# Kernel optimization log

Hardware: AMD Instinct MI355X
Metric: run time of the kernel (lower is better)

Reference implementation:

```python
import jax, jax.numpy as jnp
import numpy as np

KH, KW = 3, 3  # window_size[1], window_size[2]
SH, SW = 1, 1  # strides
FILTERS = 64


def _extract_patches(x, kh, kw, sh, sw):
    # TF tf.image.extract_patches ordering: depth = (row, col, channel), channel fastest.
    B, H, W, C = x.shape
    Ho = (H - kh) // sh + 1
    Wo = (W - kw) // sw + 1
    # stack kh*kw shifted views -> (B, Ho, Wo, kh*kw, C)
    views = [x[:, i:i + (Ho - 1) * sh + 1:sh, j:j + (Wo - 1) * sw + 1:sw, :]
             for i in range(kh) for j in range(kw)]
    patches = jnp.stack(views, axis=3)
    return patches.reshape(B, Ho, Wo, kh * kw * C)


def setup_inputs() -> dict:
    key = jax.random.key(0)
    k1, k2 = jax.random.split(key)
    B, H, W, C = 8, 32, 32, 32
    K = KH * KW * C  # 288
    x = jax.random.normal(k1, (B, H, W, C), dtype=jnp.float32)
    w = jax.random.normal(k2, (1, 1, 1, K, FILTERS), dtype=jnp.float32) * 0.05
    bias = jnp.zeros((FILTERS,), dtype=jnp.float32)
    return {"x": x, "w": w, "bias": bias}


def reference(x, w, bias):
    # patches: (B, Ho, Wo, K)
    patches = _extract_patches(x, KH, KW, SH, SW)
    # broadcast add: (B, Ho, Wo, K, F)
    s = patches[..., None] + w
    # tropical max-plus minus min-plus over the patch axis, plus bias
    return jnp.max(s, axis=3) - jnp.min(s, axis=3) + bias
```

## Files before the change

### kernel.cpp

```cpp
#include <hip/hip_runtime.h>
#include <math.h>


#define PIX 2
#define TPB 256

__global__ __launch_bounds__(TPB) void trop_kernel(
    const float* __restrict__ x,
    const float* __restrict__ w,
    const float* __restrict__ bias,
    float* __restrict__ out)
{
    __shared__ float wlds[2][32 * 64];

    const int tid  = threadIdx.x;
    const int lane = tid & 63;
    const int wv   = tid >> 6;

    const int pix0 = blockIdx.x * (4 * PIX) + wv * PIX;

    const float* xp[PIX];
#pragma unroll
    for (int p = 0; p < PIX; ++p) {
        const int pid = pix0 + p;
        const int wo = pid % 30;
        const int t  = pid / 30;
        const int ho = t % 30;
        const int b  = t / 30;
        xp[p] = x + (((b * 32 + ho) * 32) + wo) * 32;
    }

    float amax[PIX], amin[PIX];
#pragma unroll
    for (int p = 0; p < PIX; ++p) { amax[p] = -INFINITY; amin[p] = INFINITY; }

    {
        const float4* src = (const float4*)w;
        ((float4*)wlds[0])[tid]       = src[tid];
        ((float4*)wlds[0])[tid + 256] = src[tid + 256];
    }
    __syncthreads();

#pragma unroll
    for (int tap = 0; tap < 9; ++tap) {
        const int cur = tap & 1;
        const int nxt = cur ^ 1;

        const int ntap = (tap < 8) ? tap + 1 : 8;
        const float4* src = (const float4*)(w + ntap * 2048);
        const float4 r0 = src[tid];
        const float4 r1 = src[tid + 256];

        const int dy = tap / 3;
        const int dx = tap % 3;
        const int xoff = (dy * 32 + dx) * 32;

#pragma unroll
        for (int c = 0; c < 32; c += 4) {
            const float w0 = wlds[cur][(c + 0) * 64 + lane];
            const float w1 = wlds[cur][(c + 1) * 64 + lane];
            const float w2 = wlds[cur][(c + 2) * 64 + lane];
            const float w3 = wlds[cur][(c + 3) * 64 + lane];
#pragma unroll
            for (int p = 0; p < PIX; ++p) {
                const float4 xv = *(const float4*)(xp[p] + xoff + c);
                const float s0 = xv.x + w0;
                const float s1 = xv.y + w1;
                const float s2 = xv.z + w2;
                const float s3 = xv.w + w3;
                amax[p] = fmaxf(fmaxf(fmaxf(fmaxf(amax[p], s0), s1), s2), s3);
                amin[p] = fminf(fminf(fminf(fminf(amin[p], s0), s1), s2), s3);
            }
        }

        ((float4*)wlds[nxt])[tid]       = r0;
        ((float4*)wlds[nxt])[tid + 256] = r1;
        __syncthreads();
    }

    const float bv = bias[lane];
#pragma unroll
    for (int p = 0; p < PIX; ++p)
        out[(pix0 + p) * 64 + lane] = amax[p] - amin[p] + bv;
}

extern "C" void kernel_launch(void* const* d_in, const int* in_sizes, int n_in,
                              void* d_out, int out_size, void* d_ws, size_t ws_size,
                              hipStream_t stream) {
    const float* x    = (const float*)d_in[0];
    const float* w    = (const float*)d_in[1];
    const float* bias = (const float*)d_in[2];
    float* out = (float*)d_out;

    trop_kernel<<<dim3(900), dim3(TPB), 0, stream>>>(x, w, bias, out);
}
```

Baseline: 77.50 us.

## Stage weights in two large LDS phases with 512-thread blocks

```diff
diff --git a/kernel.cpp b/kernel.cpp
--- a/kernel.cpp
+++ b/kernel.cpp
@@ -2,8 +2,48 @@
 #include <math.h>
 
 
+#define TPB 512
 #define PIX 2
-#define TPB 256
+#define NTA 5
+#define NTB 4
+
+__device__ __forceinline__ float fmax3(float a, float b, float c) {
+    return fmaxf(fmaxf(a, b), c);
+}
+__device__ __forceinline__ float fmin3(float a, float b, float c) {
+    return fminf(fminf(a, b), c);
+}
+
+template <int T0, int NT>
+__device__ __forceinline__ void compute_taps(
+    const float* __restrict__ wl, const float* const* xp, int lane,
+    float* amax, float* amin)
+{
+#pragma unroll
+    for (int t = 0; t < NT; ++t) {
+        const int tap = T0 + t;
+        const int dy = tap / 3;
+        const int dx = tap % 3;
+        const int xoff = (dy * 32 + dx) * 32;
+#pragma unroll
+        for (int c = 0; c < 32; c += 4) {
+            const float w0 = wl[t * 2048 + (c + 0) * 64 + lane];
+            const float w1 = wl[t * 2048 + (c + 1) * 64 + lane];
+            const float w2 = wl[t * 2048 + (c + 2) * 64 + lane];
+            const float w3 = wl[t * 2048 + (c + 3) * 64 + lane];
+#pragma unroll
+            for (int p = 0; p < PIX; ++p) {
+                const float4 xv = *(const float4*)(xp[p] + xoff + c);
+                const float s0 = xv.x + w0;
+                const float s1 = xv.y + w1;
+                const float s2 = xv.z + w2;
+                const float s3 = xv.w + w3;
+                amax[p] = fmax3(amax[p], fmax3(s0, s1, s2), s3);
+                amin[p] = fmin3(amin[p], fmin3(s0, s1, s2), s3);
+            }
+        }
+    }
+}
 
 __global__ __launch_bounds__(TPB) void trop_kernel(
     const float* __restrict__ x,
@@ -11,13 +51,13 @@
     const float* __restrict__ bias,
     float* __restrict__ out)
 {
-    __shared__ float wlds[2][32 * 64];
+    __shared__ float wlds[NTA * 2048];
 
     const int tid  = threadIdx.x;
     const int lane = tid & 63;
     const int wv   = tid >> 6;
 
-    const int pix0 = blockIdx.x * (4 * PIX) + wv * PIX;
+    const int pix0 = blockIdx.x * (8 * PIX) + wv * PIX;
 
     const float* xp[PIX];
 #pragma unroll
@@ -30,53 +70,35 @@
         xp[p] = x + (((b * 32 + ho) * 32) + wo) * 32;
     }
 
+    {
+        const float4* src = (const float4*)w;
+        float4* dst = (float4*)wlds;
+#pragma unroll
+        for (int i = 0; i < 5; ++i) dst[tid + i * 512] = src[tid + i * 512];
+    }
+    float4 rB[4];
+    {
+        const float4* src = (const float4*)(w + NTA * 2048);
+#pragma unroll
+        for (int i = 0; i < 4; ++i) rB[i] = src[tid + i * 512];
+    }
+    __syncthreads();
+
     float amax[PIX], amin[PIX];
 #pragma unroll
     for (int p = 0; p < PIX; ++p) { amax[p] = -INFINITY; amin[p] = INFINITY; }
 
+    compute_taps<0, NTA>(wlds, xp, lane, amax, amin);
+
+    __syncthreads();
     {
-        const float4* src = (const float4*)w;
-        ((float4*)wlds[0])[tid]       = src[tid];
-        ((float4*)wlds[0])[tid + 256] = src[tid + 256];
+        float4* dst = (float4*)wlds;
+#pragma unroll
+        for (int i = 0; i < 4; ++i) dst[tid + i * 512] = rB[i];
     }
     __syncthreads();
 
-#pragma unroll
-    for (int tap = 0; tap < 9; ++tap) {
-        const int cur = tap & 1;
-        const int nxt = cur ^ 1;
-
-        const int ntap = (tap < 8) ? tap + 1 : 8;
-        const float4* src = (const float4*)(w + ntap * 2048);
-        const float4 r0 = src[tid];
-        const float4 r1 = src[tid + 256];
-
-        const int dy = tap / 3;
-        const int dx = tap % 3;
-        const int xoff = (dy * 32 + dx) * 32;
-
-#pragma unroll
-        for (int c = 0; c < 32; c += 4) {
-            const float w0 = wlds[cur][(c + 0) * 64 + lane];
-            const float w1 = wlds[cur][(c + 1) * 64 + lane];
-            const float w2 = wlds[cur][(c + 2) * 64 + lane];
-            const float w3 = wlds[cur][(c + 3) * 64 + lane];
-#pragma unroll
-            for (int p = 0; p < PIX; ++p) {
-                const float4 xv = *(const float4*)(xp[p] + xoff + c);
-                const float s0 = xv.x + w0;
-                const float s1 = xv.y + w1;
-                const float s2 = xv.z + w2;
-                const float s3 = xv.w + w3;
-                amax[p] = fmaxf(fmaxf(fmaxf(fmaxf(amax[p], s0), s1), s2), s3);
-                amin[p] = fminf(fminf(fminf(fminf(amin[p], s0), s1), s2), s3);
-            }
-        }
-
-        ((float4*)wlds[nxt])[tid]       = r0;
-        ((float4*)wlds[nxt])[tid + 256] = r1;
-        __syncthreads();
-    }
+    compute_taps<NTA, NTB>(wlds, xp, lane, amax, amin);
 
     const float bv = bias[lane];
 #pragma unroll
@@ -92,5 +114,5 @@
     const float* bias = (const float*)d_in[2];
     float* out = (float*)d_out;
 
-    trop_kernel<<<dim3(900), dim3(TPB), 0, stream>>>(x, w, bias, out);
+    trop_kernel<<<dim3(450), dim3(TPB), 0, stream>>>(x, w, bias, out);
 }
```

New measurement: 81.42 us. +5.1%, slower.
